# Kernel tuning notes

Measured on AMD Instinct MI355X. Metric: run time of the kernel, lower is better.

## Reference

```python
import jax, jax.numpy as jnp
import numpy as np

N, E, G = 50000, 800000, 64        # nodes, edges, graphs in batch
IN, HID, OUT = 64, 128, 8


def gcn_conv(x, W, b, src, dst, num_nodes):
    """GCNConv: h = D^-1/2 (A+I) D^-1/2 (x W) + b, self-loops already in src/dst."""
    h = x @ W                                              # [N, out]
    deg = jax.ops.segment_sum(jnp.ones_like(dst, dtype=h.dtype), dst,
                              num_segments=num_nodes)      # [N]
    dinv = jax.lax.rsqrt(jnp.maximum(deg, 1.0))
    norm = dinv[src] * dinv[dst]                           # [E+N]
    msg = h[src] * norm[:, None]                           # gather + scale
    out = jax.ops.segment_sum(msg, dst, num_segments=num_nodes)
    return out + b


def global_mean_pool(x, batch, num_graphs):
    s = jax.ops.segment_sum(x, batch, num_segments=num_graphs)
    cnt = jax.ops.segment_sum(jnp.ones((x.shape[0],), x.dtype), batch,
                              num_segments=num_graphs)
    return s / jnp.maximum(cnt, 1.0)[:, None]


def setup_inputs() -> dict:
    key = jax.random.key(0)
    ks = jax.random.split(key, 11)
    def glorot(k, fi, fo):
        return jax.random.normal(k, (fi, fo), jnp.float32) * np.float32(1.0 / np.sqrt(fi))
    return {
        "x": jax.random.normal(ks[0], (N, IN), jnp.float32),
        "W1": glorot(ks[1], IN, HID),  "b1": jnp.zeros((HID,), jnp.float32),
        "W2": glorot(ks[2], HID, HID), "b2": jnp.zeros((HID,), jnp.float32),
        "W3": glorot(ks[3], HID, HID), "b3": jnp.zeros((HID,), jnp.float32),
        "Wh": glorot(ks[4], HID, OUT), "bh": jnp.zeros((OUT,), jnp.float32),
        "edge_index": jax.random.randint(ks[5], (2, E), 0, N),
        "batch": jnp.sort(jax.random.randint(ks[6], (N,), 0, G)),
    }


def reference(x, W1, b1, W2, b2, W3, b3, Wh, bh, edge_index, batch):
    loops = jnp.arange(N, dtype=edge_index.dtype)
    src = jnp.concatenate([edge_index[0], loops])          # add self-loops
    dst = jnp.concatenate([edge_index[1], loops])
    h = jax.nn.relu(gcn_conv(x, W1, b1, src, dst, N))
    h = jax.nn.relu(gcn_conv(h, W2, b2, src, dst, N))
    h = gcn_conv(h, W3, b3, src, dst, N)
    g = global_mean_pool(h, batch, G)                      # [G, HID]
    return g @ Wh + bh                                     # [G, OUT]
```

## Files before the change

kernel.cpp:

```cpp
#include <hip/hip_runtime.h>

typedef short bf8_t __attribute__((ext_vector_type(8)));
typedef float f32x4 __attribute__((ext_vector_type(4)));
typedef unsigned short u16;

__device__ inline u16 f2bf(float f) {
    unsigned u = __float_as_uint(f);
    return (u16)((u + 0x7fff + ((u >> 16) & 1)) >> 16);
}


__global__ void deg_kernel(const int* __restrict__ dst, int* __restrict__ deg,
                           u16* __restrict__ rank, int E) {
    int e = blockIdx.x * 256 + threadIdx.x;
    if (e < E) rank[e] = (u16)atomicAdd(&deg[dst[e]], 1);
}

__global__ void scan_blocksum(const int* __restrict__ deg, int* __restrict__ bsum,
                              float* __restrict__ dinv, int n) {
    int i = blockIdx.x * 256 + threadIdx.x;
    int d = (i < n) ? (deg[i] + 1) : 0;
    if (i < n) dinv[i] = rsqrtf((float)d);
    int v = d;
    for (int off = 32; off > 0; off >>= 1) v += __shfl_down(v, off, 64);
    __shared__ int ws[4];
    if ((threadIdx.x & 63) == 0) ws[threadIdx.x >> 6] = v;
    __syncthreads();
    if (threadIdx.x == 0) bsum[blockIdx.x] = ws[0] + ws[1] + ws[2] + ws[3];
}

__global__ void scan_offsets(const int* __restrict__ bsum, int* __restrict__ boff, int nblk) {
    __shared__ int buf[256];
    int tid = threadIdx.x;
    int v = (tid < nblk) ? bsum[tid] : 0;
    buf[tid] = v;
    __syncthreads();
    for (int off = 1; off < 256; off <<= 1) {
        int t = (tid >= off) ? buf[tid - off] : 0;
        __syncthreads();
        buf[tid] += t;
        __syncthreads();
    }
    if (tid < nblk) boff[tid] = buf[tid] - v;
}

__global__ void scan_rowptr(const int* __restrict__ deg, const int* __restrict__ boff,
                            int* __restrict__ row_ptr, int n) {
    __shared__ int buf[256];
    int tid = threadIdx.x;
    int i = blockIdx.x * 256 + tid;
    int v = (i < n) ? (deg[i] + 1) : 0;
    buf[tid] = v;
    __syncthreads();
    for (int off = 1; off < 256; off <<= 1) {
        int t = (tid >= off) ? buf[tid - off] : 0;
        __syncthreads();
        buf[tid] += t;
        __syncthreads();
    }
    int excl = buf[tid] - v + boff[blockIdx.x];
    if (i < n) row_ptr[i] = excl;
    if (i == n - 1) row_ptr[n] = excl + v;
}

__global__ void fill_kernel(const int* __restrict__ src, const int* __restrict__ dst,
                            const u16* __restrict__ rank,
                            const int* __restrict__ row_ptr,
                            u16* __restrict__ csr_src, int E, int n) {
    int e = blockIdx.x * 256 + threadIdx.x;
    if (e < E) {
        int s = src[e], d = dst[e];
        int pos = row_ptr[d] + 1 + (int)rank[e];
        __builtin_nontemporal_store((u16)s, &csr_src[pos]);
    } else if (e < E + n) {
        int s = e - E;
        __builtin_nontemporal_store((u16)s, &csr_src[row_ptr[s]]);
    }
}

__global__ void x2bf_kernel(const float* __restrict__ x, const float* __restrict__ dinv,
                            unsigned* __restrict__ x16, int total8) {
    int i = blockIdx.x * 256 + threadIdx.x;
    if (i >= total8) return;
    float dn = dinv[i >> 3];
    const float4* x4 = (const float4*)x;
    float4 a = x4[i * 2], b = x4[i * 2 + 1];
    uint4 o;
    o.x = (unsigned)f2bf(a.x * dn) | ((unsigned)f2bf(a.y * dn) << 16);
    o.y = (unsigned)f2bf(a.z * dn) | ((unsigned)f2bf(a.w * dn) << 16);
    o.z = (unsigned)f2bf(b.x * dn) | ((unsigned)f2bf(b.y * dn) << 16);
    o.w = (unsigned)f2bf(b.z * dn) | ((unsigned)f2bf(b.w * dn) << 16);
    ((uint4*)x16)[i] = o;
}

__global__ void wt_all(const float* __restrict__ W1, const float* __restrict__ W2,
                       const float* __restrict__ W3,
                       u16* __restrict__ Wt1, u16* __restrict__ Wt2,
                       u16* __restrict__ Wt3) {
    int i = blockIdx.x * 256 + threadIdx.x;
    if (i < 8192) {
        int nn = i / 64, k = i - nn * 64;
        Wt1[i] = f2bf(W1[k * 128 + nn]);
    } else if (i < 24576) {
        int j = i - 8192;
        int nn = j / 128, k = j - nn * 128;
        Wt2[j] = f2bf(W2[k * 128 + nn]);
    } else if (i < 40960) {
        int j = i - 24576;
        int nn = j / 128, k = j - nn * 128;
        Wt3[j] = f2bf(W3[k * 128 + nn]);
    }
}


__device__ inline void bf8_add(uint4 a, float* acc) {
#pragma unroll
    for (int j = 0; j < 4; ++j) {
        unsigned u = ((const unsigned*)&a)[j];
        acc[2 * j]     += __uint_as_float(u << 16);
        acc[2 * j + 1] += __uint_as_float(u & 0xffff0000u);
    }
}

__device__ inline uint4 pack_bf8(const float* v, float dn) {
    uint4 o;
    o.x = (unsigned)f2bf(v[0] * dn) | ((unsigned)f2bf(v[1] * dn) << 16);
    o.y = (unsigned)f2bf(v[2] * dn) | ((unsigned)f2bf(v[3] * dn) << 16);
    o.z = (unsigned)f2bf(v[4] * dn) | ((unsigned)f2bf(v[5] * dn) << 16);
    o.w = (unsigned)f2bf(v[6] * dn) | ((unsigned)f2bf(v[7] * dn) << 16);
    return o;
}

template<int K, bool RELU, bool BF16OUT>
__global__ __launch_bounds__(256) void agg_gemm(
        const u16* __restrict__ in, const u16* __restrict__ Wt16,
        const float* __restrict__ bias, void* __restrict__ outp,
        const int* __restrict__ row_ptr, const u16* __restrict__ csr_src,
        const float* __restrict__ dinv, int n) {
    constexpr int KS = K / 32;
    __shared__ u16 As[16 * K];
    int w = threadIdx.x >> 6, lane = threadIdx.x & 63;
    int base = blockIdx.x * 16;
    int lr = lane & 15, lk = lane >> 4;

    bf8_t B[2][KS];
#pragma unroll
    for (int f = 0; f < 2; ++f) {
        int col = w * 32 + f * 16 + lr;
#pragma unroll
        for (int ks = 0; ks < KS; ++ks)
            B[f][ks] = *reinterpret_cast<const bf8_t*>(&Wt16[(size_t)col * K + ks * 32 + lk * 8]);
    }

    const uint4* in4 = (const uint4*)in;
    int g = lane >> 4;
    int row = w * 4 + g;
    int node = base + row;
    float acc[8] = {0.f, 0.f, 0.f, 0.f, 0.f, 0.f, 0.f, 0.f};

    if (K == 128) {
        int col = lane & 15;
        if (node < n) {
            int beg = row_ptr[node], end = row_ptr[node + 1];
            int i = beg;
            int s0 = csr_src[i], s1 = csr_src[i + 1];
            for (; i + 1 < end; i += 2) {
                int t0 = csr_src[i + 2], t1 = csr_src[i + 3];
                uint4 a = in4[(size_t)s0 * 16 + col];
                uint4 b = in4[(size_t)s1 * 16 + col];
                bf8_add(a, acc);
                bf8_add(b, acc);
                s0 = t0; s1 = t1;
            }
            if (i < end) bf8_add(in4[(size_t)s0 * 16 + col], acc);
        }
        float dn = (node < n) ? dinv[node] : 0.f;
        int off = row * K + ((col * 8) ^ ((row & 7) << 3));
        *(uint4*)&As[off] = pack_bf8(acc, dn);
    } else {
        int sub = (lane >> 3) & 1;
        int col = lane & 7;
        if (node < n) {
            int beg = row_ptr[node], end = row_ptr[node + 1];
            int i = beg + sub;
            int s0 = csr_src[i], s1 = csr_src[i + 2];
            for (; i + 2 < end; i += 4) {
                int t0 = csr_src[i + 4], t1 = csr_src[i + 6];
                uint4 a = in4[(size_t)s0 * 8 + col];
                uint4 b = in4[(size_t)s1 * 8 + col];
                bf8_add(a, acc);
                bf8_add(b, acc);
                s0 = t0; s1 = t1;
            }
            if (i < end) bf8_add(in4[(size_t)s0 * 8 + col], acc);
        }
#pragma unroll
        for (int j = 0; j < 8; ++j)
            acc[j] += __shfl_xor(acc[j], 8, 64);
        if (sub == 0) {
            float dn = (node < n) ? dinv[node] : 0.f;
            int off = row * K + ((col * 8) ^ ((row & 7) << 3));
            *(uint4*)&As[off] = pack_bf8(acc, dn);
        }
    }
    __syncthreads();

    f32x4 pacc[2] = {};
#pragma unroll
    for (int ks = 0; ks < KS; ++ks) {
        int off = lr * K + (((ks * 32) + lk * 8) ^ ((lr & 7) << 3));
        bf8_t a = *reinterpret_cast<const bf8_t*>(&As[off]);
#pragma unroll
        for (int f = 0; f < 2; ++f)
            pacc[f] = __builtin_amdgcn_mfma_f32_16x16x32_bf16(B[f][ks], a, pacc[f], 0, 0, 0);
    }

    int orow = base + lr;
    if (orow < n) {
        float dnx = BF16OUT ? dinv[orow] : 1.f;
#pragma unroll
        for (int f = 0; f < 2; ++f) {
            int c0 = w * 32 + f * 16 + lk * 4;
            float4 bv = *(const float4*)&bias[c0];
            float v0 = pacc[f][0] + bv.x, v1 = pacc[f][1] + bv.y;
            float v2 = pacc[f][2] + bv.z, v3 = pacc[f][3] + bv.w;
            if (RELU) {
                v0 = fmaxf(v0, 0.f); v1 = fmaxf(v1, 0.f);
                v2 = fmaxf(v2, 0.f); v3 = fmaxf(v3, 0.f);
            }
            if (BF16OUT) {
                uint2 o;
                o.x = (unsigned)f2bf(v0 * dnx) | ((unsigned)f2bf(v1 * dnx) << 16);
                o.y = (unsigned)f2bf(v2 * dnx) | ((unsigned)f2bf(v3 * dnx) << 16);
                *(uint2*)&((u16*)outp)[(size_t)orow * 128 + c0] = o;
            } else {
                *(float4*)&((float*)outp)[(size_t)orow * 128 + c0] = make_float4(v0, v1, v2, v3);
            }
        }
    }
}


__device__ inline int lbound(const int* __restrict__ batch, int n, int g) {
    int lo = 0, hi = n;
    while (lo < hi) {
        int mid = (lo + hi) >> 1;
        if (batch[mid] < g) lo = mid + 1; else hi = mid;
    }
    return lo;
}

#define PSPLIT 16
__global__ __launch_bounds__(256) void pool_part(
        const float* __restrict__ h, const int* __restrict__ batch,
        float* __restrict__ part, int n) {
    int g = blockIdx.x >> 4, sp = blockIdx.x & (PSPLIT - 1);
    int tid = threadIdx.x;
    int c = tid & 127, rs = tid >> 7;
    int beg = lbound(batch, n, g), end = lbound(batch, n, g + 1);
    int len = end - beg;
    int chunk = (len + PSPLIT - 1) >> 4;
    int r0 = beg + sp * chunk;
    int r1 = min(r0 + chunk, end);
    float acc = 0.f;
    for (int r = r0 + rs; r < r1; r += 2)
        acc += h[(size_t)r * 128 + c];
    __shared__ float buf[256];
    buf[tid] = acc;
    __syncthreads();
    if (rs == 0)
        part[(size_t)blockIdx.x * 128 + c] = buf[c] + buf[c + 128];
}

__global__ __launch_bounds__(128) void pool_final(
        const float* __restrict__ part, const int* __restrict__ batch,
        float* __restrict__ gout, int n) {
    int g = blockIdx.x;
    int c = threadIdx.x;
    float acc = 0.f;
#pragma unroll
    for (int sp = 0; sp < PSPLIT; ++sp)
        acc += part[((size_t)g * PSPLIT + sp) * 128 + c];
    int cnt = lbound(batch, n, g + 1) - lbound(batch, n, g);
    gout[g * 128 + c] = acc / fmaxf((float)cnt, 1.f);
}

__global__ void head_kernel(const float* __restrict__ g, const float* __restrict__ Wh,
                            const float* __restrict__ bh, float* __restrict__ out, int G) {
    int tid = blockIdx.x * blockDim.x + threadIdx.x;
    if (tid >= G * 8) return;
    int gi = tid >> 3, o = tid & 7;
    float acc = bh[o];
    for (int k = 0; k < 128; ++k)
        acc = fmaf(g[gi * 128 + k], Wh[k * 8 + o], acc);
    out[tid] = acc;
}


extern "C" void kernel_launch(void* const* d_in, const int* in_sizes, int n_in,
                              void* d_out, int out_size, void* d_ws, size_t ws_size,
                              hipStream_t stream) {
    const float* x  = (const float*)d_in[0];
    const float* W1 = (const float*)d_in[1];
    const float* b1 = (const float*)d_in[2];
    const float* W2 = (const float*)d_in[3];
    const float* b2 = (const float*)d_in[4];
    const float* W3 = (const float*)d_in[5];
    const float* b3 = (const float*)d_in[6];
    const float* Wh = (const float*)d_in[7];
    const float* bh = (const float*)d_in[8];
    const int* edge_index = (const int*)d_in[9];
    const int* batch = (const int*)d_in[10];
    (void)n_in; (void)ws_size;

    const int N = in_sizes[10];
    const int E = in_sizes[9] / 2;
    const int G = out_size / 8;
    const int* esrc = edge_index;
    const int* edst = edge_index + E;

    size_t off = 0;
    auto take = [&](size_t bytes) {
        void* p = (char*)d_ws + off;
        off += (bytes + 255) & ~(size_t)255;
        return p;
    };
    int*   deg      = (int*)take((size_t)N * 4);
    float* dinv     = (float*)take((size_t)N * 4);
    int*   row_ptr  = (int*)take((size_t)(N + 1) * 4);
    u16*   rank     = (u16*)take((size_t)E * 2);
    u16*   csr_src  = (u16*)take((size_t)(E + N + 64) * 2);
    int*   bsum     = (int*)take(256 * 4);
    int*   boff     = (int*)take(256 * 4);
    float* part     = (float*)take((size_t)G * PSPLIT * 128 * 4);
    float* gpool    = (float*)take((size_t)G * 128 * 4);
    u16*   x16      = (u16*)take((size_t)N * 64 * 2);
    u16*   h16a     = (u16*)take((size_t)N * 128 * 2);
    u16*   h16b     = (u16*)take((size_t)N * 128 * 2);
    u16*   Wt1      = (u16*)take((size_t)128 * 64 * 2);
    u16*   Wt2      = (u16*)take((size_t)128 * 128 * 2);
    u16*   Wt3      = (u16*)take((size_t)128 * 128 * 2);
    float* bufA     = (float*)take((size_t)N * 128 * 4);

    int nblk = (N + 255) / 256;
    int fgrid = (N + 15) / 16;

    hipMemsetAsync(deg, 0, (size_t)N * 4, stream);

    deg_kernel<<<(E + 255) / 256, 256, 0, stream>>>(edst, deg, rank, E);
    scan_blocksum<<<nblk, 256, 0, stream>>>(deg, bsum, dinv, N);
    scan_offsets<<<1, 256, 0, stream>>>(bsum, boff, nblk);
    scan_rowptr<<<nblk, 256, 0, stream>>>(deg, boff, row_ptr, N);
    fill_kernel<<<(E + N + 255) / 256, 256, 0, stream>>>(esrc, edst, rank, row_ptr, csr_src, E, N);
    x2bf_kernel<<<(N * 64 / 8 + 255) / 256, 256, 0, stream>>>(x, dinv, (unsigned*)x16, N * 64 / 8);
    wt_all<<<(40960 + 255) / 256, 256, 0, stream>>>(W1, W2, W3, Wt1, Wt2, Wt3);

    agg_gemm<64,  true,  true ><<<fgrid, 256, 0, stream>>>(x16,  Wt1, b1, h16a, row_ptr, csr_src, dinv, N);
    agg_gemm<128, true,  true ><<<fgrid, 256, 0, stream>>>(h16a, Wt2, b2, h16b, row_ptr, csr_src, dinv, N);
    agg_gemm<128, false, false><<<fgrid, 256, 0, stream>>>(h16b, Wt3, b3, bufA, row_ptr, csr_src, dinv, N);

    pool_part<<<G * PSPLIT, 256, 0, stream>>>(bufA, batch, part, N);
    pool_final<<<G, 128, 0, stream>>>(part, batch, gpool, N);
    head_kernel<<<(G * 8 + 255) / 256, 256, 0, stream>>>(gpool, Wh, bh, (float*)d_out, G);
}
```

Measured before the change: 224.5 us.

## Sort nodes by degree to balance per-wave gather work in aggregation

Adds a three-kernel counting sort that buckets nodes by in-degree (capped at 64 bins) into a permutation array. Each aggregate-GEMM block then processes 16 nodes of similar degree, so the four rows in a wave have matching loop trip counts and less divergence. The cost is three extra small launches plus indirect node lookups. Output rows are now scattered rather than contiguous, and gather locality changes with the new order.

```diff
diff --git a/kernel.cpp b/kernel.cpp
--- a/kernel.cpp
+++ b/kernel.cpp
@@ -76,6 +76,52 @@
         int s = e - E;
         __builtin_nontemporal_store((u16)s, &csr_src[row_ptr[s]]);
     }
+}
+
+#define NBIN 64
+
+__global__ void sortA(const int* __restrict__ deg, int* __restrict__ blockhist,
+                      u16* __restrict__ lrank, int n, int nblk) {
+    __shared__ int h[NBIN];
+    int tid = threadIdx.x;
+    if (tid < NBIN) h[tid] = 0;
+    __syncthreads();
+    int i = blockIdx.x * 256 + tid;
+    if (i < n) {
+        int b = min(deg[i], NBIN - 1);
+        lrank[i] = (u16)atomicAdd(&h[b], 1);
+    }
+    __syncthreads();
+    if (tid < NBIN) blockhist[tid * nblk + blockIdx.x] = h[tid];
+}
+
+__global__ void sortB(int* __restrict__ blockhist, int* __restrict__ binoff, int nblk) {
+    __shared__ int tot[NBIN];
+    int b = threadIdx.x;
+    if (b < NBIN) {
+        int run = 0;
+#pragma unroll 8
+        for (int k = 0; k < nblk; ++k) {
+            int t = blockhist[b * nblk + k];
+            blockhist[b * nblk + k] = run;
+            run += t;
+        }
+        tot[b] = run;
+    }
+    __syncthreads();
+    if (b == 0) {
+        int run = 0;
+        for (int k = 0; k < NBIN; ++k) { binoff[k] = run; run += tot[k]; }
+    }
+}
+
+__global__ void sortC(const int* __restrict__ deg, const u16* __restrict__ lrank,
+                      const int* __restrict__ blockhist, const int* __restrict__ binoff,
+                      int* __restrict__ perm, int n, int nblk) {
+    int i = blockIdx.x * 256 + threadIdx.x;
+    if (i >= n) return;
+    int b = min(deg[i], NBIN - 1);
+    perm[binoff[b] + blockhist[b * nblk + blockIdx.x] + (int)lrank[i]] = i;
 }
 
 __global__ void x2bf_kernel(const float* __restrict__ x, const float* __restrict__ dinv,
@@ -136,7 +182,7 @@
         const u16* __restrict__ in, const u16* __restrict__ Wt16,
         const float* __restrict__ bias, void* __restrict__ outp,
         const int* __restrict__ row_ptr, const u16* __restrict__ csr_src,
-        const float* __restrict__ dinv, int n) {
+        const float* __restrict__ dinv, const int* __restrict__ perm, int n) {
     constexpr int KS = K / 32;
     __shared__ u16 As[16 * K];
     int w = threadIdx.x >> 6, lane = threadIdx.x & 63;
@@ -155,12 +201,13 @@
     const uint4* in4 = (const uint4*)in;
     int g = lane >> 4;
     int row = w * 4 + g;
-    int node = base + row;
+    int prow = base + row;
+    int node = (prow < n) ? perm[prow] : -1;
     float acc[8] = {0.f, 0.f, 0.f, 0.f, 0.f, 0.f, 0.f, 0.f};
 
     if (K == 128) {
         int col = lane & 15;
-        if (node < n) {
+        if (node >= 0) {
             int beg = row_ptr[node], end = row_ptr[node + 1];
             int i = beg;
             int s0 = csr_src[i], s1 = csr_src[i + 1];
@@ -174,13 +221,13 @@
             }
             if (i < end) bf8_add(in4[(size_t)s0 * 16 + col], acc);
         }
-        float dn = (node < n) ? dinv[node] : 0.f;
+        float dn = (node >= 0) ? dinv[node] : 0.f;
         int off = row * K + ((col * 8) ^ ((row & 7) << 3));
         *(uint4*)&As[off] = pack_bf8(acc, dn);
     } else {
         int sub = (lane >> 3) & 1;
         int col = lane & 7;
-        if (node < n) {
+        if (node >= 0) {
             int beg = row_ptr[node], end = row_ptr[node + 1];
             int i = beg + sub;
             int s0 = csr_src[i], s1 = csr_src[i + 2];
@@ -198,7 +245,7 @@
         for (int j = 0; j < 8; ++j)
             acc[j] += __shfl_xor(acc[j], 8, 64);
         if (sub == 0) {
-            float dn = (node < n) ? dinv[node] : 0.f;
+            float dn = (node >= 0) ? dinv[node] : 0.f;
             int off = row * K + ((col * 8) ^ ((row & 7) << 3));
             *(uint4*)&As[off] = pack_bf8(acc, dn);
         }
@@ -215,9 +262,10 @@
             pacc[f] = __builtin_amdgcn_mfma_f32_16x16x32_bf16(B[f][ks], a, pacc[f], 0, 0, 0);
     }
 
-    int orow = base + lr;
-    if (orow < n) {
-        float dnx = BF16OUT ? dinv[orow] : 1.f;
+    int oprow = base + lr;
+    if (oprow < n) {
+        int onode = perm[oprow];
+        float dnx = BF16OUT ? dinv[onode] : 1.f;
 #pragma unroll
         for (int f = 0; f < 2; ++f) {
             int c0 = w * 32 + f * 16 + lk * 4;
@@ -232,9 +280,9 @@
                 uint2 o;
                 o.x = (unsigned)f2bf(v0 * dnx) | ((unsigned)f2bf(v1 * dnx) << 16);
                 o.y = (unsigned)f2bf(v2 * dnx) | ((unsigned)f2bf(v3 * dnx) << 16);
-                *(uint2*)&((u16*)outp)[(size_t)orow * 128 + c0] = o;
+                *(uint2*)&((u16*)outp)[(size_t)onode * 128 + c0] = o;
             } else {
-                *(float4*)&((float*)outp)[(size_t)orow * 128 + c0] = make_float4(v0, v1, v2, v3);
+                *(float4*)&((float*)outp)[(size_t)onode * 128 + c0] = make_float4(v0, v1, v2, v3);
             }
         }
     }
@@ -325,6 +373,7 @@
         off += (bytes + 255) & ~(size_t)255;
         return p;
     };
+    int nblk = (N + 255) / 256;
     int*   deg      = (int*)take((size_t)N * 4);
     float* dinv     = (float*)take((size_t)N * 4);
     int*   row_ptr  = (int*)take((size_t)(N + 1) * 4);
@@ -332,6 +381,10 @@
     u16*   csr_src  = (u16*)take((size_t)(E + N + 64) * 2);
     int*   bsum     = (int*)take(256 * 4);
     int*   boff     = (int*)take(256 * 4);
+    int*   blockhist= (int*)take((size_t)NBIN * nblk * 4);
+    int*   binoff   = (int*)take(NBIN * 4);
+    u16*   lrank    = (u16*)take((size_t)N * 2);
+    int*   perm     = (int*)take((size_t)N * 4);
     float* part     = (float*)take((size_t)G * PSPLIT * 128 * 4);
     float* gpool    = (float*)take((size_t)G * 128 * 4);
     u16*   x16      = (u16*)take((size_t)N * 64 * 2);
@@ -342,7 +395,6 @@
     u16*   Wt3      = (u16*)take((size_t)128 * 128 * 2);
     float* bufA     = (float*)take((size_t)N * 128 * 4);
 
-    int nblk = (N + 255) / 256;
     int fgrid = (N + 15) / 16;
 
     hipMemsetAsync(deg, 0, (size_t)N * 4, stream);
@@ -352,12 +404,15 @@
     scan_offsets<<<1, 256, 0, stream>>>(bsum, boff, nblk);
     scan_rowptr<<<nblk, 256, 0, stream>>>(deg, boff, row_ptr, N);
     fill_kernel<<<(E + N + 255) / 256, 256, 0, stream>>>(esrc, edst, rank, row_ptr, csr_src, E, N);
+    sortA<<<nblk, 256, 0, stream>>>(deg, blockhist, lrank, N, nblk);
+    sortB<<<1, 256, 0, stream>>>(blockhist, binoff, nblk);
+    sortC<<<nblk, 256, 0, stream>>>(deg, lrank, blockhist, binoff, perm, N, nblk);
     x2bf_kernel<<<(N * 64 / 8 + 255) / 256, 256, 0, stream>>>(x, dinv, (unsigned*)x16, N * 64 / 8);
     wt_all<<<(40960 + 255) / 256, 256, 0, stream>>>(W1, W2, W3, Wt1, Wt2, Wt3);
 
-    agg_gemm<64,  true,  true ><<<fgrid, 256, 0, stream>>>(x16,  Wt1, b1, h16a, row_ptr, csr_src, dinv, N);
-    agg_gemm<128, true,  true ><<<fgrid, 256, 0, stream>>>(h16a, Wt2, b2, h16b, row_ptr, csr_src, dinv, N);
-    agg_gemm<128, false, false><<<fgrid, 256, 0, stream>>>(h16b, Wt3, b3, bufA, row_ptr, csr_src, dinv, N);
+    agg_gemm<64,  true,  true ><<<fgrid, 256, 0, stream>>>(x16,  Wt1, b1, h16a, row_ptr, csr_src, dinv, perm, N);
+    agg_gemm<128, true,  true ><<<fgrid, 256, 0, stream>>>(h16a, Wt2, b2, h16b, row_ptr, csr_src, dinv, perm, N);
+    agg_gemm<128, false, false><<<fgrid, 256, 0, stream>>>(h16b, Wt3, b3, bufA, row_ptr, csr_src, dinv, perm, N);
 
     pool_part<<<G * PSPLIT, 256, 0, stream>>>(bufA, batch, part, N);
     pool_final<<<G, 128, 0, stream>>>(part, batch, gpool, N);
```

After: 236.9 us. 1.06x slower.
